# Performance work log

Hardware: AMD Instinct MI355X
Metric: run time of the kernel (lower is better)

Reference implementation:

```python
import jax, jax.numpy as jnp
import numpy as np

N = 200_000           # particles
E = 6_400_000         # neighbor pairs (~32 per particle)
SUPPORT = 0.05
EPS = SUPPORT ** 2 * 0.1
DELTA = 0.1
C0 = 10.0 * float(np.sqrt(2.0 * 9.81 * 0.3))
REST_DENSITY = 1000.0
_KC = 7.0 / float(np.pi)  # 2D Wendland C2 normalization


def kernel_gradient(q, dirs, h):
    # Wendland C2 (2D): W = C/h^2 (1-q)^4 (1+4q), q = r/h in [0,1]
    # dW/dr = C/h^3 * (-20 q (1-q)^3), directed along unit vector dirs
    dkdq = -20.0 * q * (1.0 - q) ** 3 * _KC
    return dirs * (dkdq / h ** 3)[:, None]


def setup_inputs() -> dict:
    key = jax.random.key(0)
    k = jax.random.split(key, 7)
    i = jnp.sort(jax.random.randint(k[0], (E,), 0, N))
    j = jax.random.randint(k[1], (E,), 0, N)
    fluidPosition = jax.random.uniform(k[2], (N, 2), dtype=jnp.float32)
    dx2 = (SUPPORT * 0.5) ** 2
    fluidVolume = dx2 * (1.0 + 0.01 * jax.random.normal(k[3], (N,), dtype=jnp.float32))
    fluidDensity = 0.95 + 0.1 * jax.random.uniform(k[4], (N,), dtype=jnp.float32)
    d = jax.random.normal(k[5], (E, 2), dtype=jnp.float32)
    distances = d / (jnp.linalg.norm(d, axis=1, keepdims=True) + 1e-8)  # unit directions
    radialDistances = jax.random.uniform(k[6], (E,), dtype=jnp.float32, minval=0.05, maxval=1.0)
    return {"fluidPosition": fluidPosition, "fluidVolume": fluidVolume,
            "fluidDensity": fluidDensity, "distances": distances,
            "radialDistances": radialDistances, "i": i, "j": j}


def reference(fluidPosition, fluidVolume, fluidDensity, distances, radialDistances, i, j):
    h = SUPPORT
    n = fluidDensity.shape[0]
    gradW = kernel_gradient(radialDistances, distances, h)          # [E,2]
    r_ba = -distances * (radialDistances * h)[:, None]              # [E,2] displacement
    Vj = fluidVolume[j]

    # --- normalization matrix: sum_j 2 Vj * outer(r_ba, gradW) ---
    term = jnp.einsum('nu,nv->nuv', r_ba, gradW) * (2.0 * Vj)[:, None, None]
    M = jax.ops.segment_sum(term, i, num_segments=n)                # [N,2,2]

    # --- pseudo-inverse + renormalized kernel gradient per edge ---
    Li = jnp.linalg.pinv(M)                                         # [N,2,2]
    grad = jnp.einsum('nuv,nv->nu', Li[i], gradW)                   # [E,2]
    dwij_mag = jnp.sum(jnp.abs(gradW), axis=1)                      # L1 norms
    norm_mag = jnp.sum(jnp.abs(grad), axis=1)
    change = jnp.abs(norm_mag - dwij_mag) / (dwij_mag + 1e-4 * h)
    grad = jnp.where((change < 0.1)[:, None], grad, gradW)

    # --- renormalized density gradient ---
    rho = fluidDensity * REST_DENSITY
    rho_ba = rho[j] - rho[i]
    gradRho = jax.ops.segment_sum((2.0 * rho_ba * Vj)[:, None] * grad, i, num_segments=n)

    # --- deltaSPH density diffusion ---
    rji2 = jnp.sum(r_ba * r_ba, axis=1) + EPS
    densityTerm = 0.5 * jnp.einsum('nu,nu->n', gradRho[i] + gradRho[j], r_ba)
    gradTerm = jnp.einsum('nu,nu->n', gradW, r_ba / rji2[:, None])
    prod = (rho_ba + densityTerm) * gradTerm
    return 2.0 * h * DELTA * C0 * jax.ops.segment_sum(prod * Vj, i, num_segments=n)
```

## Files before the change

### kernel.cpp

```cpp
#include <hip/hip_runtime.h>
#include <math.h>

#define WAVE 64

#define KC        2.2281692032865347f
#define H         0.05f
#define INV_H2    400.0f
#define INV_H3    8000.0f
#define EPS_REF   0.00025f
#define K_OUT     0.24261080f
#define REST_RHO  1000.0f

__device__ __forceinline__ float wendland_dkdq(float q) {
    float omq = 1.0f - q;
    return -20.0f * q * omq * omq * omq * KC;
}

template<int NV>
__device__ __forceinline__ void seg_reduce4(const int k[4], float v[4][NV],
                                            float* __restrict__ base) {
    const int lane = threadIdx.x & (WAVE - 1);
    const int k0 = k[0], k3 = k[3];
    const bool split = (k0 != k3);
    const int firstLen  = (k[1]==k0) ? ((k[2]==k0) ? ((k[3]==k0)?4:3) : 2) : 1;
    const int lastStart = (k[2]==k3) ? ((k[1]==k3) ? ((k[0]==k3)?0:1) : 2) : 3;

    float vin[NV], vfirst[NV];
#pragma unroll
    for (int c = 0; c < NV; ++c) {
        float s = v[3][c];
        if (lastStart <= 2) s += v[2][c];
        if (lastStart <= 1) s += v[1][c];
        if (lastStart == 0) s += v[0][c];
        vin[c] = s;
        float f = v[0][c];
        if (firstLen >= 2) f += v[1][c];
        if (firstLen >= 3) f += v[2][c];
        if (firstLen >= 4) f += v[3][c];
        vfirst[c] = f;
    }

#pragma unroll
    for (int idx = 1; idx <= 2; ++idx) {
        if (idx >= firstLen && idx < lastStart && k[idx] >= 0) {
#pragma unroll
            for (int c = 0; c < NV; ++c)
                atomicAdd(base + (size_t)k[idx] * NV + c, v[idx][c]);
        }
    }

    float S[NV];
#pragma unroll
    for (int c = 0; c < NV; ++c) S[c] = vin[c];
    const int klast = k3;
#pragma unroll
    for (int d = 1; d < WAVE; d <<= 1) {
        int okey = __shfl_up(klast, d, WAVE);
        float ov[NV];
#pragma unroll
        for (int c = 0; c < NV; ++c) ov[c] = __shfl_up(S[c], d, WAVE);
        if (lane >= d && okey == klast) {
#pragma unroll
            for (int c = 0; c < NV; ++c) S[c] += ov[c];
        }
    }

    const int prevk = __shfl_up(klast, 1, WAVE);
    float P[NV];
#pragma unroll
    for (int c = 0; c < NV; ++c) P[c] = __shfl_up(S[c], 1, WAVE);
    if (split && k0 >= 0) {
        const bool carry = (lane > 0 && prevk == k0);
#pragma unroll
        for (int c = 0; c < NV; ++c)
            atomicAdd(base + (size_t)k0 * NV + c, vfirst[c] + (carry ? P[c] : 0.f));
    }

    const int nk0 = __shfl_down(k0, 1, WAVE);
    const bool tail = (lane == WAVE - 1) || (nk0 != klast);
    if (tail && klast >= 0) {
#pragma unroll
        for (int c = 0; c < NV; ++c)
            atomicAdd(base + (size_t)klast * NV + c, S[c]);
    }
}

struct Edge4 {
    int   i[4], j[4];
    float q[4], dx[4], dy[4];
};

__device__ __forceinline__ void load_edge4(int t, int E,
        const int* __restrict__ ei, const int* __restrict__ ej,
        const float* __restrict__ qarr, const float2* __restrict__ dirs, Edge4& ed) {
    const long e0 = 4L * t;
    if (e0 + 3 < (long)E) {
        int4   i4 = ((const int4*)ei)[t];
        int4   j4 = ((const int4*)ej)[t];
        float4 q4 = ((const float4*)qarr)[t];
        float4 dA = ((const float4*)dirs)[2 * t];
        float4 dB = ((const float4*)dirs)[2 * t + 1];
        ed.i[0]=i4.x; ed.i[1]=i4.y; ed.i[2]=i4.z; ed.i[3]=i4.w;
        ed.j[0]=j4.x; ed.j[1]=j4.y; ed.j[2]=j4.z; ed.j[3]=j4.w;
        ed.q[0]=q4.x; ed.q[1]=q4.y; ed.q[2]=q4.z; ed.q[3]=q4.w;
        ed.dx[0]=dA.x; ed.dy[0]=dA.y; ed.dx[1]=dA.z; ed.dy[1]=dA.w;
        ed.dx[2]=dB.x; ed.dy[2]=dB.y; ed.dx[3]=dB.z; ed.dy[3]=dB.w;
    } else {
        int lastk = -1;
#pragma unroll
        for (int u = 0; u < 4; ++u) {
            long e = e0 + u;
            if (e < (long)E) {
                ed.i[u] = ei[e]; ed.j[u] = ej[e]; ed.q[u] = qarr[e];
                float2 d = dirs[e]; ed.dx[u] = d.x; ed.dy[u] = d.y;
                lastk = ed.i[u];
            } else {
                ed.i[u] = lastk; ed.j[u] = 0; ed.q[u] = 0.f;
                ed.dx[u] = 0.f; ed.dy[u] = 0.f;
            }
        }
    }
}

__global__ void k_edge_M4(const float2* __restrict__ dirs, const float* __restrict__ qarr,
                          const int* __restrict__ ei, const int* __restrict__ ej,
                          const float* __restrict__ vol, float* __restrict__ M, int E) {
    int t = blockIdx.x * blockDim.x + threadIdx.x;
    Edge4 ed; load_edge4(t, E, ei, ej, qarr, dirs, ed);
    float vj[4];
#pragma unroll
    for (int u = 0; u < 4; ++u) vj[u] = vol[ed.j[u]];
    int k[4]; float v[4][3];
#pragma unroll
    for (int u = 0; u < 4; ++u) {
        float q = ed.q[u];
        float s = -2.0f * vj[u] * q * wendland_dkdq(q) * INV_H2;
        k[u] = ed.i[u];
        v[u][0] = s * ed.dx[u] * ed.dx[u];
        v[u][1] = s * ed.dx[u] * ed.dy[u];
        v[u][2] = s * ed.dy[u] * ed.dy[u];
    }
    seg_reduce4<3>(k, v, M);
}

__global__ void k_node_pinv_pack(float* __restrict__ M, const float* __restrict__ vol,
                                 const float* __restrict__ dens, float2* __restrict__ vd, int N) {
    int n = blockIdx.x * blockDim.x + threadIdx.x;
    if (n >= N) return;
    vd[n] = make_float2(vol[n], dens[n]);
    float a = M[3*n+0], b = M[3*n+1], c = M[3*n+2];
    float half_tr   = 0.5f * (a + c);
    float half_diff = 0.5f * (a - c);
    float disc = sqrtf(half_diff * half_diff + b * b);
    float l1 = half_tr + disc, l2 = half_tr - disc;
    float smax = fmaxf(fabsf(l1), fabsf(l2));
    float cutoff = 2.3841858e-6f * smax;
    float i00 = 0.f, i01 = 0.f, i11 = 0.f;
    if (fabsf(l2) > cutoff) {
        float inv = 1.0f / (a * c - b * b);
        i00 =  c * inv; i01 = -b * inv; i11 = a * inv;
    } else if (fabsf(l1) > cutoff) {
        float vax = b,      vay = l1 - a;
        float vbx = l1 - c, vby = b;
        float na = vax*vax + vay*vay, nb = vbx*vbx + vby*vby;
        float vx, vy, n2;
        if (nb >= na) { vx = vbx; vy = vby; n2 = nb; }
        else          { vx = vax; vy = vay; n2 = na; }
        float inv = 1.0f / (l1 * n2);
        i00 = vx*vx*inv; i01 = vx*vy*inv; i11 = vy*vy*inv;
    }
    M[3*n+0] = i00; M[3*n+1] = i01; M[3*n+2] = i11;
}

__global__ void k_edge_gradRho4(const float2* __restrict__ dirs, const float* __restrict__ qarr,
                                const int* __restrict__ ei, const int* __restrict__ ej,
                                const float2* __restrict__ vd, const float* __restrict__ Li,
                                float* __restrict__ gradRho, int E) {
    int t = blockIdx.x * blockDim.x + threadIdx.x;
    Edge4 ed; load_edge4(t, E, ei, ej, qarr, dirs, ed);
    float2 vdj[4];
#pragma unroll
    for (int u = 0; u < 4; ++u) vdj[u] = vd[ed.j[u]];
    int k[4]; float v[4][2];
#pragma unroll
    for (int u = 0; u < 4; ++u) {
        int key = ed.i[u];
        k[u] = key;
        v[u][0] = 0.f; v[u][1] = 0.f;
        if (key >= 0) {
            float q = ed.q[u];
            float w = wendland_dkdq(q) * INV_H3;
            float gwx = ed.dx[u] * w, gwy = ed.dy[u] * w;
            float li00 = Li[3*key+0], li01 = Li[3*key+1], li11 = Li[3*key+2];
            float gx = li00 * gwx + li01 * gwy;
            float gy = li01 * gwx + li11 * gwy;
            float dwij_mag = fabsf(gwx) + fabsf(gwy);
            float norm_mag = fabsf(gx) + fabsf(gy);
            float change = fabsf(norm_mag - dwij_mag) / (dwij_mag + 1e-4f * H);
            if (!(change < 0.1f)) { gx = gwx; gy = gwy; }
            float dens_i = vd[key].y;
            float val = 2.0f * REST_RHO * (vdj[u].y - dens_i) * vdj[u].x;
            v[u][0] = val * gx;
            v[u][1] = val * gy;
        }
    }
    seg_reduce4<2>(k, v, gradRho);
}

__global__ void k_pack_nd(const float* __restrict__ vol, const float* __restrict__ dens,
                          const float2* __restrict__ gradRho, float4* __restrict__ nd, int N) {
    int n = blockIdx.x * blockDim.x + threadIdx.x;
    if (n >= N) return;
    float2 g = gradRho[n];
    nd[n] = make_float4(vol[n], dens[n], g.x, g.y);
}

__global__ void k_edge_out4(const float2* __restrict__ dirs, const float* __restrict__ qarr,
                            const int* __restrict__ ei, const int* __restrict__ ej,
                            const float4* __restrict__ nd, float* __restrict__ out, int E) {
    int t = blockIdx.x * blockDim.x + threadIdx.x;
    Edge4 ed; load_edge4(t, E, ei, ej, qarr, dirs, ed);
    float4 ndj[4];
#pragma unroll
    for (int u = 0; u < 4; ++u) ndj[u] = nd[ed.j[u]];
    int k[4]; float v[4][1];
#pragma unroll
    for (int u = 0; u < 4; ++u) {
        int key = ed.i[u];
        k[u] = key;
        v[u][0] = 0.f;
        if (key >= 0) {
            float4 ndi = nd[key];
            float q = ed.q[u];
            float w = wendland_dkdq(q) * INV_H3;
            float gwx = ed.dx[u] * w, gwy = ed.dy[u] * w;
            float rx = -ed.dx[u] * q * H, ry = -ed.dy[u] * q * H;
            float rji2 = rx * rx + ry * ry + EPS_REF;
            float gradTerm = (gwx * rx + gwy * ry) / rji2;
            float densityTerm = 0.5f * ((ndi.z + ndj[u].z) * rx + (ndi.w + ndj[u].w) * ry);
            float rho_ba = REST_RHO * (ndj[u].y - ndi.y);
            v[u][0] = (rho_ba + densityTerm) * gradTerm * ndj[u].x * K_OUT;
        }
    }
    seg_reduce4<1>(k, v, out);
}

extern "C" void kernel_launch(void* const* d_in, const int* in_sizes, int n_in,
                              void* d_out, int out_size, void* d_ws, size_t ws_size,
                              hipStream_t stream) {
    const float*  vol  = (const float*)d_in[1];
    const float*  dens = (const float*)d_in[2];
    const float2* dirs = (const float2*)d_in[3];
    const float*  qarr = (const float*)d_in[4];
    const int*    ei   = (const int*)d_in[5];
    const int*    ej   = (const int*)d_in[6];
    const int N = in_sizes[1];
    const int E = in_sizes[4];

    float*  M       = (float*)d_ws;
    float*  gradRho = M + (size_t)N * 3;
    float2* vd      = (float2*)(M + (size_t)N * 5);
    float4* nd      = (float4*)(M + (size_t)N * 7);
    float*  out     = (float*)d_out;

    hipMemsetAsync(M, 0, (size_t)N * 5 * sizeof(float), stream);
    hipMemsetAsync(out, 0, (size_t)N * sizeof(float), stream);

    const int tb = 256;
    const int T  = (E + 3) / 4;
    const int gE = (T + tb - 1) / tb;
    const int gN = (N + tb - 1) / tb;

    k_edge_M4       <<<gE, tb, 0, stream>>>(dirs, qarr, ei, ej, vol, M, E);
    k_node_pinv_pack<<<gN, tb, 0, stream>>>(M, vol, dens, vd, N);
    k_edge_gradRho4 <<<gE, tb, 0, stream>>>(dirs, qarr, ei, ej, vd, M, gradRho, E);
    k_pack_nd       <<<gN, tb, 0, stream>>>(vol, dens, (const float2*)gradRho, nd, N);
    k_edge_out4     <<<gE, tb, 0, stream>>>(dirs, qarr, ei, ej, nd, out, E);
}
```

Before: 289.6 us.

## Cache per-edge directions and Vj/density-diff as half2 to cut gathers

The first edge pass now also writes per-edge half-precision copies of the unit direction and of (Vj, rho_j - rho_i). Later passes read these streamed 8 bytes per edge instead of the fp32 directions plus random gathers of neighbor volume and density. The pseudo-inverse is stored as float4 for a single aligned load, and the node packing kernels are merged. This trades random gathers and fp32 traffic for extra edge writes and fp16 rounding of directions and volumes. The density differences (up to about 100) also lose precision in half, which may exceed tolerance. A fallback path is used when the workspace is too small.

```diff
diff --git a/kernel.cpp b/kernel.cpp
--- a/kernel.cpp
+++ b/kernel.cpp
@@ -1,4 +1,5 @@
 #include <hip/hip_runtime.h>
+#include <hip/hip_fp16.h>
 #include <math.h>
 
 #define WAVE 64
@@ -15,6 +16,10 @@
     float omq = 1.0f - q;
     return -20.0f * q * omq * omq * omq * KC;
 }
+
+union H2F { __half2 h; float f; };
+__device__ __forceinline__ float   h2_as_f(__half2 h) { H2F u; u.h = h; return u.f; }
+__device__ __forceinline__ __half2 f_as_h2(float f)   { H2F u; u.f = f; return u.h; }
 
 template<int NV>
 __device__ __forceinline__ void seg_reduce4(const int k[4], float v[4][NV],
@@ -39,7 +44,6 @@
         if (firstLen >= 4) f += v[3][c];
         vfirst[c] = f;
     }
-
 #pragma unroll
     for (int idx = 1; idx <= 2; ++idx) {
         if (idx >= firstLen && idx < lastStart && k[idx] >= 0) {
@@ -48,7 +52,6 @@
                 atomicAdd(base + (size_t)k[idx] * NV + c, v[idx][c]);
         }
     }
-
     float S[NV];
 #pragma unroll
     for (int c = 0; c < NV; ++c) S[c] = vin[c];
@@ -64,7 +67,6 @@
             for (int c = 0; c < NV; ++c) S[c] += ov[c];
         }
     }
-
     const int prevk = __shfl_up(klast, 1, WAVE);
     float P[NV];
 #pragma unroll
@@ -75,7 +77,6 @@
         for (int c = 0; c < NV; ++c)
             atomicAdd(base + (size_t)k0 * NV + c, vfirst[c] + (carry ? P[c] : 0.f));
     }
-
     const int nk0 = __shfl_down(k0, 1, WAVE);
     const bool tail = (lane == WAVE - 1) || (nk0 != klast);
     if (tail && klast >= 0) {
@@ -85,69 +86,83 @@
     }
 }
 
-struct Edge4 {
-    int   i[4], j[4];
-    float q[4], dx[4], dy[4];
-};
-
-__device__ __forceinline__ void load_edge4(int t, int E,
-        const int* __restrict__ ei, const int* __restrict__ ej,
-        const float* __restrict__ qarr, const float2* __restrict__ dirs, Edge4& ed) {
-    const long e0 = 4L * t;
+__global__ void k_init(const float* __restrict__ vol, const float* __restrict__ dens,
+                       float2* __restrict__ vd, int N) {
+    int n = blockIdx.x * blockDim.x + threadIdx.x;
+    if (n < N) vd[n] = make_float2(vol[n], dens[n]);
+}
+
+template<bool FULL>
+__global__ void k_A(const int* __restrict__ ei, const int* __restrict__ ej,
+                    const float* __restrict__ qarr, const float2* __restrict__ dirs,
+                    const float2* __restrict__ vd, __half2* __restrict__ ehd,
+                    __half2* __restrict__ vr, float* __restrict__ M, int E) {
+    int t = blockIdx.x * blockDim.x + threadIdx.x;
+    long e0 = 4L * t;
+    int k[4]; float v[4][3];
     if (e0 + 3 < (long)E) {
         int4   i4 = ((const int4*)ei)[t];
         int4   j4 = ((const int4*)ej)[t];
         float4 q4 = ((const float4*)qarr)[t];
         float4 dA = ((const float4*)dirs)[2 * t];
         float4 dB = ((const float4*)dirs)[2 * t + 1];
-        ed.i[0]=i4.x; ed.i[1]=i4.y; ed.i[2]=i4.z; ed.i[3]=i4.w;
-        ed.j[0]=j4.x; ed.j[1]=j4.y; ed.j[2]=j4.z; ed.j[3]=j4.w;
-        ed.q[0]=q4.x; ed.q[1]=q4.y; ed.q[2]=q4.z; ed.q[3]=q4.w;
-        ed.dx[0]=dA.x; ed.dy[0]=dA.y; ed.dx[1]=dA.z; ed.dy[1]=dA.w;
-        ed.dx[2]=dB.x; ed.dy[2]=dB.y; ed.dx[3]=dB.z; ed.dy[3]=dB.w;
+        int   iv[4] = {i4.x, i4.y, i4.z, i4.w};
+        int   jv[4] = {j4.x, j4.y, j4.z, j4.w};
+        float qv[4] = {q4.x, q4.y, q4.z, q4.w};
+        float dxv[4] = {dA.x, dA.z, dB.x, dB.z};
+        float dyv[4] = {dA.y, dA.w, dB.y, dB.w};
+        float2 vdj[4];
+#pragma unroll
+        for (int u = 0; u < 4; ++u) vdj[u] = vd[jv[u]];
+        float4 ehp, vrp;
+#pragma unroll
+        for (int u = 0; u < 4; ++u) {
+            float rhoi = vd[iv[u]].y;
+            float q = qv[u], dx = dxv[u], dy = dyv[u];
+            float Vj = vdj[u].x;
+            float dro = vdj[u].y - rhoi;
+            float s = -2.0f * Vj * q * wendland_dkdq(q) * INV_H2;
+            k[u] = iv[u];
+            v[u][0] = s * dx * dx; v[u][1] = s * dx * dy; v[u][2] = s * dy * dy;
+            if (FULL) {
+                (&ehp.x)[u] = h2_as_f(__floats2half2_rn(dx, dy));
+                (&vrp.x)[u] = h2_as_f(__floats2half2_rn(Vj, dro));
+            }
+        }
+        if (FULL) {
+            ((float4*)ehd)[t] = ehp;
+            ((float4*)vr)[t]  = vrp;
+        }
     } else {
         int lastk = -1;
 #pragma unroll
         for (int u = 0; u < 4; ++u) {
             long e = e0 + u;
             if (e < (long)E) {
-                ed.i[u] = ei[e]; ed.j[u] = ej[e]; ed.q[u] = qarr[e];
-                float2 d = dirs[e]; ed.dx[u] = d.x; ed.dy[u] = d.y;
-                lastk = ed.i[u];
+                int ii = ei[e], jj = ej[e];
+                float q = qarr[e];
+                float2 d = dirs[e];
+                float2 vdj = vd[jj];
+                float dro = vdj.y - vd[ii].y;
+                float s = -2.0f * vdj.x * q * wendland_dkdq(q) * INV_H2;
+                k[u] = ii;
+                v[u][0] = s * d.x * d.x; v[u][1] = s * d.x * d.y; v[u][2] = s * d.y * d.y;
+                if (FULL) {
+                    ehd[e] = __floats2half2_rn(d.x, d.y);
+                    vr[e]  = __floats2half2_rn(vdj.x, dro);
+                }
+                lastk = ii;
             } else {
-                ed.i[u] = lastk; ed.j[u] = 0; ed.q[u] = 0.f;
-                ed.dx[u] = 0.f; ed.dy[u] = 0.f;
-            }
-        }
-    }
-}
-
-__global__ void k_edge_M4(const float2* __restrict__ dirs, const float* __restrict__ qarr,
-                          const int* __restrict__ ei, const int* __restrict__ ej,
-                          const float* __restrict__ vol, float* __restrict__ M, int E) {
-    int t = blockIdx.x * blockDim.x + threadIdx.x;
-    Edge4 ed; load_edge4(t, E, ei, ej, qarr, dirs, ed);
-    float vj[4];
-#pragma unroll
-    for (int u = 0; u < 4; ++u) vj[u] = vol[ed.j[u]];
-    int k[4]; float v[4][3];
-#pragma unroll
-    for (int u = 0; u < 4; ++u) {
-        float q = ed.q[u];
-        float s = -2.0f * vj[u] * q * wendland_dkdq(q) * INV_H2;
-        k[u] = ed.i[u];
-        v[u][0] = s * ed.dx[u] * ed.dx[u];
-        v[u][1] = s * ed.dx[u] * ed.dy[u];
-        v[u][2] = s * ed.dy[u] * ed.dy[u];
+                k[u] = lastk; v[u][0] = v[u][1] = v[u][2] = 0.f;
+            }
+        }
     }
     seg_reduce4<3>(k, v, M);
 }
 
-__global__ void k_node_pinv_pack(float* __restrict__ M, const float* __restrict__ vol,
-                                 const float* __restrict__ dens, float2* __restrict__ vd, int N) {
+__global__ void k_pinv(const float* __restrict__ M, float4* __restrict__ Li4, int N) {
     int n = blockIdx.x * blockDim.x + threadIdx.x;
     if (n >= N) return;
-    vd[n] = make_float2(vol[n], dens[n]);
     float a = M[3*n+0], b = M[3*n+1], c = M[3*n+2];
     float half_tr   = 0.5f * (a + c);
     float half_diff = 0.5f * (a - c);
@@ -169,77 +184,184 @@
         float inv = 1.0f / (l1 * n2);
         i00 = vx*vx*inv; i01 = vx*vy*inv; i11 = vy*vy*inv;
     }
-    M[3*n+0] = i00; M[3*n+1] = i01; M[3*n+2] = i11;
-}
-
-__global__ void k_edge_gradRho4(const float2* __restrict__ dirs, const float* __restrict__ qarr,
-                                const int* __restrict__ ei, const int* __restrict__ ej,
-                                const float2* __restrict__ vd, const float* __restrict__ Li,
-                                float* __restrict__ gradRho, int E) {
+    Li4[n] = make_float4(i00, i01, i11, 0.f);
+}
+
+template<bool FULL>
+__global__ void k_C(const int* __restrict__ ei, const int* __restrict__ ej,
+                    const float* __restrict__ qarr, const float2* __restrict__ dirs,
+                    const __half2* __restrict__ ehd, const __half2* __restrict__ vr,
+                    const float2* __restrict__ vd, const float4* __restrict__ Li4,
+                    float* __restrict__ g, int E) {
     int t = blockIdx.x * blockDim.x + threadIdx.x;
-    Edge4 ed; load_edge4(t, E, ei, ej, qarr, dirs, ed);
-    float2 vdj[4];
-#pragma unroll
-    for (int u = 0; u < 4; ++u) vdj[u] = vd[ed.j[u]];
+    long e0 = 4L * t;
     int k[4]; float v[4][2];
-#pragma unroll
-    for (int u = 0; u < 4; ++u) {
-        int key = ed.i[u];
-        k[u] = key;
-        v[u][0] = 0.f; v[u][1] = 0.f;
-        if (key >= 0) {
-            float q = ed.q[u];
+    if (e0 + 3 < (long)E) {
+        int4   i4 = ((const int4*)ei)[t];
+        float4 q4 = ((const float4*)qarr)[t];
+        int   iv[4] = {i4.x, i4.y, i4.z, i4.w};
+        float qv[4] = {q4.x, q4.y, q4.z, q4.w};
+        float dxv[4], dyv[4], Vjv[4], drov[4];
+        if (FULL) {
+            float4 es = ((const float4*)ehd)[t];
+            float4 vs = ((const float4*)vr)[t];
+#pragma unroll
+            for (int u = 0; u < 4; ++u) {
+                __half2 hd = f_as_h2((&es.x)[u]);
+                __half2 hv = f_as_h2((&vs.x)[u]);
+                dxv[u] = __low2float(hd);  dyv[u] = __high2float(hd);
+                Vjv[u] = __low2float(hv);  drov[u] = __high2float(hv);
+            }
+        } else {
+            int4   j4 = ((const int4*)ej)[t];
+            float4 dA = ((const float4*)dirs)[2 * t];
+            float4 dB = ((const float4*)dirs)[2 * t + 1];
+            int jv[4] = {j4.x, j4.y, j4.z, j4.w};
+            dxv[0]=dA.x; dyv[0]=dA.y; dxv[1]=dA.z; dyv[1]=dA.w;
+            dxv[2]=dB.x; dyv[2]=dB.y; dxv[3]=dB.z; dyv[3]=dB.w;
+#pragma unroll
+            for (int u = 0; u < 4; ++u) {
+                float2 vdj = vd[jv[u]];
+                Vjv[u] = vdj.x; drov[u] = vdj.y - vd[iv[u]].y;
+            }
+        }
+#pragma unroll
+        for (int u = 0; u < 4; ++u) {
+            int key = iv[u]; k[u] = key;
+            float q = qv[u];
             float w = wendland_dkdq(q) * INV_H3;
-            float gwx = ed.dx[u] * w, gwy = ed.dy[u] * w;
-            float li00 = Li[3*key+0], li01 = Li[3*key+1], li11 = Li[3*key+2];
-            float gx = li00 * gwx + li01 * gwy;
-            float gy = li01 * gwx + li11 * gwy;
+            float gwx = dxv[u] * w, gwy = dyv[u] * w;
+            float4 L = Li4[key];
+            float gx = L.x * gwx + L.y * gwy;
+            float gy = L.y * gwx + L.z * gwy;
             float dwij_mag = fabsf(gwx) + fabsf(gwy);
             float norm_mag = fabsf(gx) + fabsf(gy);
             float change = fabsf(norm_mag - dwij_mag) / (dwij_mag + 1e-4f * H);
             if (!(change < 0.1f)) { gx = gwx; gy = gwy; }
-            float dens_i = vd[key].y;
-            float val = 2.0f * REST_RHO * (vdj[u].y - dens_i) * vdj[u].x;
+            float val = 2.0f * REST_RHO * drov[u] * Vjv[u];
             v[u][0] = val * gx;
             v[u][1] = val * gy;
         }
-    }
-    seg_reduce4<2>(k, v, gradRho);
-}
-
-__global__ void k_pack_nd(const float* __restrict__ vol, const float* __restrict__ dens,
-                          const float2* __restrict__ gradRho, float4* __restrict__ nd, int N) {
-    int n = blockIdx.x * blockDim.x + threadIdx.x;
-    if (n >= N) return;
-    float2 g = gradRho[n];
-    nd[n] = make_float4(vol[n], dens[n], g.x, g.y);
-}
-
-__global__ void k_edge_out4(const float2* __restrict__ dirs, const float* __restrict__ qarr,
-                            const int* __restrict__ ei, const int* __restrict__ ej,
-                            const float4* __restrict__ nd, float* __restrict__ out, int E) {
+    } else {
+        int lastk = -1;
+#pragma unroll
+        for (int u = 0; u < 4; ++u) {
+            long e = e0 + u;
+            v[u][0] = v[u][1] = 0.f;
+            if (e < (long)E) {
+                int key = ei[e]; lastk = key; k[u] = key;
+                float q = qarr[e];
+                float dx, dy, Vj, dro;
+                if (FULL) {
+                    __half2 hd = ehd[e], hv = vr[e];
+                    dx = __low2float(hd); dy = __high2float(hd);
+                    Vj = __low2float(hv); dro = __high2float(hv);
+                } else {
+                    float2 d = dirs[e]; dx = d.x; dy = d.y;
+                    float2 vdj = vd[ej[e]];
+                    Vj = vdj.x; dro = vdj.y - vd[key].y;
+                }
+                float w = wendland_dkdq(q) * INV_H3;
+                float gwx = dx * w, gwy = dy * w;
+                float4 L = Li4[key];
+                float gx = L.x * gwx + L.y * gwy;
+                float gy = L.y * gwx + L.z * gwy;
+                float dwij_mag = fabsf(gwx) + fabsf(gwy);
+                float norm_mag = fabsf(gx) + fabsf(gy);
+                float change = fabsf(norm_mag - dwij_mag) / (dwij_mag + 1e-4f * H);
+                if (!(change < 0.1f)) { gx = gwx; gy = gwy; }
+                float val = 2.0f * REST_RHO * dro * Vj;
+                v[u][0] = val * gx; v[u][1] = val * gy;
+            } else k[u] = lastk;
+        }
+    }
+    seg_reduce4<2>(k, v, g);
+}
+
+template<bool FULL>
+__global__ void k_D(const int* __restrict__ ei, const int* __restrict__ ej,
+                    const float* __restrict__ qarr, const float2* __restrict__ dirs,
+                    const __half2* __restrict__ ehd, const __half2* __restrict__ vr,
+                    const float2* __restrict__ vd, const float2* __restrict__ g,
+                    float* __restrict__ out, int E) {
     int t = blockIdx.x * blockDim.x + threadIdx.x;
-    Edge4 ed; load_edge4(t, E, ei, ej, qarr, dirs, ed);
-    float4 ndj[4];
-#pragma unroll
-    for (int u = 0; u < 4; ++u) ndj[u] = nd[ed.j[u]];
+    long e0 = 4L * t;
     int k[4]; float v[4][1];
-#pragma unroll
-    for (int u = 0; u < 4; ++u) {
-        int key = ed.i[u];
-        k[u] = key;
-        v[u][0] = 0.f;
-        if (key >= 0) {
-            float4 ndi = nd[key];
-            float q = ed.q[u];
+    if (e0 + 3 < (long)E) {
+        int4   i4 = ((const int4*)ei)[t];
+        int4   j4 = ((const int4*)ej)[t];
+        float4 q4 = ((const float4*)qarr)[t];
+        int   iv[4] = {i4.x, i4.y, i4.z, i4.w};
+        int   jv[4] = {j4.x, j4.y, j4.z, j4.w};
+        float qv[4] = {q4.x, q4.y, q4.z, q4.w};
+        float dxv[4], dyv[4], Vjv[4], drov[4];
+        if (FULL) {
+            float4 es = ((const float4*)ehd)[t];
+            float4 vs = ((const float4*)vr)[t];
+#pragma unroll
+            for (int u = 0; u < 4; ++u) {
+                __half2 hd = f_as_h2((&es.x)[u]);
+                __half2 hv = f_as_h2((&vs.x)[u]);
+                dxv[u] = __low2float(hd);  dyv[u] = __high2float(hd);
+                Vjv[u] = __low2float(hv);  drov[u] = __high2float(hv);
+            }
+        } else {
+            float4 dA = ((const float4*)dirs)[2 * t];
+            float4 dB = ((const float4*)dirs)[2 * t + 1];
+            dxv[0]=dA.x; dyv[0]=dA.y; dxv[1]=dA.z; dyv[1]=dA.w;
+            dxv[2]=dB.x; dyv[2]=dB.y; dxv[3]=dB.z; dyv[3]=dB.w;
+#pragma unroll
+            for (int u = 0; u < 4; ++u) {
+                float2 vdj = vd[jv[u]];
+                Vjv[u] = vdj.x; drov[u] = vdj.y - vd[iv[u]].y;
+            }
+        }
+        float2 gjv[4];
+#pragma unroll
+        for (int u = 0; u < 4; ++u) gjv[u] = g[jv[u]];
+#pragma unroll
+        for (int u = 0; u < 4; ++u) {
+            int key = iv[u]; k[u] = key;
+            float2 gi = g[key];
+            float q = qv[u];
             float w = wendland_dkdq(q) * INV_H3;
-            float gwx = ed.dx[u] * w, gwy = ed.dy[u] * w;
-            float rx = -ed.dx[u] * q * H, ry = -ed.dy[u] * q * H;
+            float gwx = dxv[u] * w, gwy = dyv[u] * w;
+            float rx = -dxv[u] * q * H, ry = -dyv[u] * q * H;
             float rji2 = rx * rx + ry * ry + EPS_REF;
             float gradTerm = (gwx * rx + gwy * ry) / rji2;
-            float densityTerm = 0.5f * ((ndi.z + ndj[u].z) * rx + (ndi.w + ndj[u].w) * ry);
-            float rho_ba = REST_RHO * (ndj[u].y - ndi.y);
-            v[u][0] = (rho_ba + densityTerm) * gradTerm * ndj[u].x * K_OUT;
+            float densityTerm = 0.5f * ((gi.x + gjv[u].x) * rx + (gi.y + gjv[u].y) * ry);
+            float rho_ba = REST_RHO * drov[u];
+            v[u][0] = (rho_ba + densityTerm) * gradTerm * Vjv[u] * K_OUT;
+        }
+    } else {
+        int lastk = -1;
+#pragma unroll
+        for (int u = 0; u < 4; ++u) {
+            long e = e0 + u;
+            v[u][0] = 0.f;
+            if (e < (long)E) {
+                int key = ei[e], jj = ej[e]; lastk = key; k[u] = key;
+                float q = qarr[e];
+                float dx, dy, Vj, dro;
+                if (FULL) {
+                    __half2 hd = ehd[e], hv = vr[e];
+                    dx = __low2float(hd); dy = __high2float(hd);
+                    Vj = __low2float(hv); dro = __high2float(hv);
+                } else {
+                    float2 d = dirs[e]; dx = d.x; dy = d.y;
+                    float2 vdj = vd[jj];
+                    Vj = vdj.x; dro = vdj.y - vd[key].y;
+                }
+                float2 gi = g[key], gj = g[jj];
+                float w = wendland_dkdq(q) * INV_H3;
+                float gwx = dx * w, gwy = dy * w;
+                float rx = -dx * q * H, ry = -dy * q * H;
+                float rji2 = rx * rx + ry * ry + EPS_REF;
+                float gradTerm = (gwx * rx + gwy * ry) / rji2;
+                float densityTerm = 0.5f * ((gi.x + gj.x) * rx + (gi.y + gj.y) * ry);
+                float rho_ba = REST_RHO * dro;
+                v[u][0] = (rho_ba + densityTerm) * gradTerm * Vj * K_OUT;
+            } else k[u] = lastk;
         }
     }
     seg_reduce4<1>(k, v, out);
@@ -257,23 +379,36 @@
     const int N = in_sizes[1];
     const int E = in_sizes[4];
 
-    float*  M       = (float*)d_ws;
-    float*  gradRho = M + (size_t)N * 3;
-    float2* vd      = (float2*)(M + (size_t)N * 5);
-    float4* nd      = (float4*)(M + (size_t)N * 7);
-    float*  out     = (float*)d_out;
-
-    hipMemsetAsync(M, 0, (size_t)N * 5 * sizeof(float), stream);
-    hipMemsetAsync(out, 0, (size_t)N * sizeof(float), stream);
+    size_t off = 0;
+    auto alloc = [&](size_t bytes) { void* r = (char*)d_ws + off;
+                                     off = (off + bytes + 15) & ~(size_t)15; return r; };
+    float2*  vd  = (float2*) alloc((size_t)N * 8);
+    float*   M   = (float*)  alloc((size_t)N * 12);
+    float4*  Li4 = (float4*) alloc((size_t)N * 16);
+    __half2* ehd = (__half2*)alloc((size_t)E * 4);
+    __half2* vr  = (__half2*)alloc((size_t)E * 4);
+    const bool full = (off <= ws_size);
+    float2*  g   = full ? vd : (float2*)M;
+    float*   out = (float*)d_out;
 
     const int tb = 256;
-    const int T  = (E + 3) / 4;
-    const int gE = (T + tb - 1) / tb;
     const int gN = (N + tb - 1) / tb;
-
-    k_edge_M4       <<<gE, tb, 0, stream>>>(dirs, qarr, ei, ej, vol, M, E);
-    k_node_pinv_pack<<<gN, tb, 0, stream>>>(M, vol, dens, vd, N);
-    k_edge_gradRho4 <<<gE, tb, 0, stream>>>(dirs, qarr, ei, ej, vd, M, gradRho, E);
-    k_pack_nd       <<<gN, tb, 0, stream>>>(vol, dens, (const float2*)gradRho, nd, N);
-    k_edge_out4     <<<gE, tb, 0, stream>>>(dirs, qarr, ei, ej, nd, out, E);
-}
+    const int gT = ((E + 3) / 4 + tb - 1) / tb;
+
+    k_init<<<gN, tb, 0, stream>>>(vol, dens, vd, N);
+    hipMemsetAsync(M, 0, (size_t)N * 12, stream);
+    hipMemsetAsync(out, 0, (size_t)N * 4, stream);
+    if (full) {
+        k_A<true><<<gT, tb, 0, stream>>>(ei, ej, qarr, dirs, vd, ehd, vr, M, E);
+        k_pinv<<<gN, tb, 0, stream>>>(M, Li4, N);
+        hipMemsetAsync(g, 0, (size_t)N * 8, stream);
+        k_C<true><<<gT, tb, 0, stream>>>(ei, ej, qarr, dirs, ehd, vr, vd, Li4, (float*)g, E);
+        k_D<true><<<gT, tb, 0, stream>>>(ei, ej, qarr, dirs, ehd, vr, vd, g, out, E);
+    } else {
+        k_A<false><<<gT, tb, 0, stream>>>(ei, ej, qarr, dirs, vd, ehd, vr, M, E);
+        k_pinv<<<gN, tb, 0, stream>>>(M, Li4, N);
+        hipMemsetAsync(g, 0, (size_t)N * 8, stream);
+        k_C<false><<<gT, tb, 0, stream>>>(ei, ej, qarr, dirs, ehd, vr, vd, Li4, (float*)g, E);
+        k_D<false><<<gT, tb, 0, stream>>>(ei, ej, qarr, dirs, ehd, vr, vd, g, out, E);
+    }
+}
```

Result: faster. 255.0 us (-12.0%).

## Fuse M, pinv and gradRho into node-blocked CSR kernel with shared-memory reductions

Applied to the files above, without the earlier changes.

Builds a CSR row pointer from the sorted i array, then has each block own 32 particles and walk their edge range. M accumulation, pseudo-inverse and gradRho reduction happen in one kernel using shared-memory atomics, and the first chunks of per-edge data are cached in registers for reuse between the two passes. This removes the global atomics, the memsets and the intermediate node kernels, and cuts edge re-reads. In exchange it adds a rowptr prep pass and extra block syncs, and per-block load balance now depends on how many edges each 32-particle group has.

```diff
diff --git a/kernel.cpp b/kernel.cpp
--- a/kernel.cpp
+++ b/kernel.cpp
@@ -1,7 +1,10 @@
 #include <hip/hip_runtime.h>
 #include <math.h>
 
-#define WAVE 64
+#define WAVE   64
+#define NPB    32
+#define BLOCKT 256
+#define SMAX   2
 
 #define KC        2.2281692032865347f
 #define H         0.05f
@@ -12,13 +15,12 @@
 #define REST_RHO  1000.0f
 
 __device__ __forceinline__ float wendland_dkdq(float q) {
-    float omq = 1.0f - q;
-    return -20.0f * q * omq * omq * omq * KC;
+    float o = 1.f - q;
+    return -20.f * q * o * o * o * KC;
 }
 
 template<int NV>
-__device__ __forceinline__ void seg_reduce4(const int k[4], float v[4][NV],
-                                            float* __restrict__ base) {
+__device__ __forceinline__ void seg_reduce4(const int k[4], float v[4][NV], float* base) {
     const int lane = threadIdx.x & (WAVE - 1);
     const int k0 = k[0], k3 = k[3];
     const bool split = (k0 != k3);
@@ -39,7 +41,6 @@
         if (firstLen >= 4) f += v[3][c];
         vfirst[c] = f;
     }
-
 #pragma unroll
     for (int idx = 1; idx <= 2; ++idx) {
         if (idx >= firstLen && idx < lastStart && k[idx] >= 0) {
@@ -48,7 +49,6 @@
                 atomicAdd(base + (size_t)k[idx] * NV + c, v[idx][c]);
         }
     }
-
     float S[NV];
 #pragma unroll
     for (int c = 0; c < NV; ++c) S[c] = vin[c];
@@ -64,7 +64,6 @@
             for (int c = 0; c < NV; ++c) S[c] += ov[c];
         }
     }
-
     const int prevk = __shfl_up(klast, 1, WAVE);
     float P[NV];
 #pragma unroll
@@ -75,7 +74,6 @@
         for (int c = 0; c < NV; ++c)
             atomicAdd(base + (size_t)k0 * NV + c, vfirst[c] + (carry ? P[c] : 0.f));
     }
-
     const int nk0 = __shfl_down(k0, 1, WAVE);
     const bool tail = (lane == WAVE - 1) || (nk0 != klast);
     if (tail && klast >= 0) {
@@ -85,164 +83,257 @@
     }
 }
 
-struct Edge4 {
-    int   i[4], j[4];
-    float q[4], dx[4], dy[4];
-};
-
-__device__ __forceinline__ void load_edge4(int t, int E,
+struct EW { int iv[4], jv[4]; float qv[4], dxv[4], dyv[4]; bool okv[4]; };
+
+__device__ __forceinline__ void load_win(long e0, int beg, int end, int E,
         const int* __restrict__ ei, const int* __restrict__ ej,
-        const float* __restrict__ qarr, const float2* __restrict__ dirs, Edge4& ed) {
-    const long e0 = 4L * t;
+        const float* __restrict__ qarr, const float2* __restrict__ dirs, EW& w) {
     if (e0 + 3 < (long)E) {
-        int4   i4 = ((const int4*)ei)[t];
-        int4   j4 = ((const int4*)ej)[t];
-        float4 q4 = ((const float4*)qarr)[t];
-        float4 dA = ((const float4*)dirs)[2 * t];
-        float4 dB = ((const float4*)dirs)[2 * t + 1];
-        ed.i[0]=i4.x; ed.i[1]=i4.y; ed.i[2]=i4.z; ed.i[3]=i4.w;
-        ed.j[0]=j4.x; ed.j[1]=j4.y; ed.j[2]=j4.z; ed.j[3]=j4.w;
-        ed.q[0]=q4.x; ed.q[1]=q4.y; ed.q[2]=q4.z; ed.q[3]=q4.w;
-        ed.dx[0]=dA.x; ed.dy[0]=dA.y; ed.dx[1]=dA.z; ed.dy[1]=dA.w;
-        ed.dx[2]=dB.x; ed.dy[2]=dB.y; ed.dx[3]=dB.z; ed.dy[3]=dB.w;
+        int4   i4 = *(const int4*)(ei + e0);
+        int4   j4 = *(const int4*)(ej + e0);
+        float4 q4 = *(const float4*)(qarr + e0);
+        float4 dA = *(const float4*)((const float*)dirs + 2 * e0);
+        float4 dB = *(const float4*)((const float*)dirs + 2 * e0 + 4);
+        w.iv[0]=i4.x; w.iv[1]=i4.y; w.iv[2]=i4.z; w.iv[3]=i4.w;
+        w.jv[0]=j4.x; w.jv[1]=j4.y; w.jv[2]=j4.z; w.jv[3]=j4.w;
+        w.qv[0]=q4.x; w.qv[1]=q4.y; w.qv[2]=q4.z; w.qv[3]=q4.w;
+        w.dxv[0]=dA.x; w.dyv[0]=dA.y; w.dxv[1]=dA.z; w.dyv[1]=dA.w;
+        w.dxv[2]=dB.x; w.dyv[2]=dB.y; w.dxv[3]=dB.z; w.dyv[3]=dB.w;
     } else {
-        int lastk = -1;
 #pragma unroll
         for (int u = 0; u < 4; ++u) {
             long e = e0 + u;
             if (e < (long)E) {
-                ed.i[u] = ei[e]; ed.j[u] = ej[e]; ed.q[u] = qarr[e];
-                float2 d = dirs[e]; ed.dx[u] = d.x; ed.dy[u] = d.y;
-                lastk = ed.i[u];
-            } else {
-                ed.i[u] = lastk; ed.j[u] = 0; ed.q[u] = 0.f;
-                ed.dx[u] = 0.f; ed.dy[u] = 0.f;
-            }
-        }
-    }
-}
-
-__global__ void k_edge_M4(const float2* __restrict__ dirs, const float* __restrict__ qarr,
-                          const int* __restrict__ ei, const int* __restrict__ ej,
-                          const float* __restrict__ vol, float* __restrict__ M, int E) {
-    int t = blockIdx.x * blockDim.x + threadIdx.x;
-    Edge4 ed; load_edge4(t, E, ei, ej, qarr, dirs, ed);
-    float vj[4];
-#pragma unroll
-    for (int u = 0; u < 4; ++u) vj[u] = vol[ed.j[u]];
-    int k[4]; float v[4][3];
+                w.iv[u] = ei[e]; w.jv[u] = ej[e]; w.qv[u] = qarr[e];
+                float2 d = dirs[e]; w.dxv[u] = d.x; w.dyv[u] = d.y;
+            } else { w.iv[u]=0; w.jv[u]=0; w.qv[u]=0.f; w.dxv[u]=0.f; w.dyv[u]=0.f; }
+        }
+    }
 #pragma unroll
     for (int u = 0; u < 4; ++u) {
-        float q = ed.q[u];
-        float s = -2.0f * vj[u] * q * wendland_dkdq(q) * INV_H2;
-        k[u] = ed.i[u];
-        v[u][0] = s * ed.dx[u] * ed.dx[u];
-        v[u][1] = s * ed.dx[u] * ed.dy[u];
-        v[u][2] = s * ed.dy[u] * ed.dy[u];
-    }
-    seg_reduce4<3>(k, v, M);
-}
-
-__global__ void k_node_pinv_pack(float* __restrict__ M, const float* __restrict__ vol,
-                                 const float* __restrict__ dens, float2* __restrict__ vd, int N) {
-    int n = blockIdx.x * blockDim.x + threadIdx.x;
-    if (n >= N) return;
-    vd[n] = make_float2(vol[n], dens[n]);
-    float a = M[3*n+0], b = M[3*n+1], c = M[3*n+2];
-    float half_tr   = 0.5f * (a + c);
-    float half_diff = 0.5f * (a - c);
-    float disc = sqrtf(half_diff * half_diff + b * b);
-    float l1 = half_tr + disc, l2 = half_tr - disc;
-    float smax = fmaxf(fabsf(l1), fabsf(l2));
-    float cutoff = 2.3841858e-6f * smax;
-    float i00 = 0.f, i01 = 0.f, i11 = 0.f;
-    if (fabsf(l2) > cutoff) {
-        float inv = 1.0f / (a * c - b * b);
-        i00 =  c * inv; i01 = -b * inv; i11 = a * inv;
-    } else if (fabsf(l1) > cutoff) {
-        float vax = b,      vay = l1 - a;
-        float vbx = l1 - c, vby = b;
-        float na = vax*vax + vay*vay, nb = vbx*vbx + vby*vby;
-        float vx, vy, n2;
-        if (nb >= na) { vx = vbx; vy = vby; n2 = nb; }
-        else          { vx = vax; vy = vay; n2 = na; }
-        float inv = 1.0f / (l1 * n2);
-        i00 = vx*vx*inv; i01 = vx*vy*inv; i11 = vy*vy*inv;
-    }
-    M[3*n+0] = i00; M[3*n+1] = i01; M[3*n+2] = i11;
-}
-
-__global__ void k_edge_gradRho4(const float2* __restrict__ dirs, const float* __restrict__ qarr,
-                                const int* __restrict__ ei, const int* __restrict__ ej,
-                                const float2* __restrict__ vd, const float* __restrict__ Li,
-                                float* __restrict__ gradRho, int E) {
-    int t = blockIdx.x * blockDim.x + threadIdx.x;
-    Edge4 ed; load_edge4(t, E, ei, ej, qarr, dirs, ed);
-    float2 vdj[4];
-#pragma unroll
-    for (int u = 0; u < 4; ++u) vdj[u] = vd[ed.j[u]];
-    int k[4]; float v[4][2];
-#pragma unroll
-    for (int u = 0; u < 4; ++u) {
-        int key = ed.i[u];
-        k[u] = key;
-        v[u][0] = 0.f; v[u][1] = 0.f;
-        if (key >= 0) {
-            float q = ed.q[u];
-            float w = wendland_dkdq(q) * INV_H3;
-            float gwx = ed.dx[u] * w, gwy = ed.dy[u] * w;
-            float li00 = Li[3*key+0], li01 = Li[3*key+1], li11 = Li[3*key+2];
-            float gx = li00 * gwx + li01 * gwy;
-            float gy = li01 * gwx + li11 * gwy;
-            float dwij_mag = fabsf(gwx) + fabsf(gwy);
-            float norm_mag = fabsf(gx) + fabsf(gy);
-            float change = fabsf(norm_mag - dwij_mag) / (dwij_mag + 1e-4f * H);
-            if (!(change < 0.1f)) { gx = gwx; gy = gwy; }
-            float dens_i = vd[key].y;
-            float val = 2.0f * REST_RHO * (vdj[u].y - dens_i) * vdj[u].x;
-            v[u][0] = val * gx;
-            v[u][1] = val * gy;
-        }
-    }
-    seg_reduce4<2>(k, v, gradRho);
-}
-
-__global__ void k_pack_nd(const float* __restrict__ vol, const float* __restrict__ dens,
-                          const float2* __restrict__ gradRho, float4* __restrict__ nd, int N) {
-    int n = blockIdx.x * blockDim.x + threadIdx.x;
-    if (n >= N) return;
-    float2 g = gradRho[n];
-    nd[n] = make_float4(vol[n], dens[n], g.x, g.y);
-}
-
-__global__ void k_edge_out4(const float2* __restrict__ dirs, const float* __restrict__ qarr,
-                            const int* __restrict__ ei, const int* __restrict__ ej,
-                            const float4* __restrict__ nd, float* __restrict__ out, int E) {
-    int t = blockIdx.x * blockDim.x + threadIdx.x;
-    Edge4 ed; load_edge4(t, E, ei, ej, qarr, dirs, ed);
-    float4 ndj[4];
-#pragma unroll
-    for (int u = 0; u < 4; ++u) ndj[u] = nd[ed.j[u]];
-    int k[4]; float v[4][1];
-#pragma unroll
-    for (int u = 0; u < 4; ++u) {
-        int key = ed.i[u];
-        k[u] = key;
-        v[u][0] = 0.f;
-        if (key >= 0) {
-            float4 ndi = nd[key];
-            float q = ed.q[u];
-            float w = wendland_dkdq(q) * INV_H3;
-            float gwx = ed.dx[u] * w, gwy = ed.dy[u] * w;
-            float rx = -ed.dx[u] * q * H, ry = -ed.dy[u] * q * H;
-            float rji2 = rx * rx + ry * ry + EPS_REF;
-            float gradTerm = (gwx * rx + gwy * ry) / rji2;
-            float densityTerm = 0.5f * ((ndi.z + ndj[u].z) * rx + (ndi.w + ndj[u].w) * ry);
-            float rho_ba = REST_RHO * (ndj[u].y - ndi.y);
-            v[u][0] = (rho_ba + densityTerm) * gradTerm * ndj[u].x * K_OUT;
-        }
-    }
-    seg_reduce4<1>(k, v, out);
+        long e = e0 + u;
+        w.okv[u] = (e >= (long)beg) && (e < (long)end) && (e < (long)E);
+    }
+}
+
+__global__ void k_prep(const int* __restrict__ ei, const float* __restrict__ vol,
+                       const float* __restrict__ dens, int* __restrict__ rowptr,
+                       float2* __restrict__ vd, int N, int E) {
+    int e = blockIdx.x * blockDim.x + threadIdx.x;
+    if (e <= E) {
+        int prev = (e == 0) ? -1 : ei[e - 1];
+        int cur  = (e == E) ? N  : ei[e];
+        for (int t = prev + 1; t <= cur; ++t) rowptr[t] = e;
+    }
+    if (e < N) vd[e] = make_float2(vol[e], dens[e]);
+}
+
+__global__ __launch_bounds__(BLOCKT, 4)
+void k_AC(const int* __restrict__ ei, const int* __restrict__ ej,
+          const float* __restrict__ qarr, const float2* __restrict__ dirs,
+          const float2* __restrict__ vd, const int* __restrict__ rowptr,
+          float4* __restrict__ nd, int N, int E) {
+    __shared__ float  Mld[NPB * 3];
+    __shared__ float  Lild[NPB * 3];
+    __shared__ float  gld[NPB * 2];
+    __shared__ float2 vdl[NPB];
+    const int tid = threadIdx.x;
+    const int n0  = blockIdx.x * NPB;
+    const int nHi = min(n0 + NPB, N);
+    if (tid < NPB && n0 + tid < N) vdl[tid] = vd[n0 + tid];
+    if (tid < NPB * 3) Mld[tid] = 0.f;
+    if (tid < NPB * 2) gld[tid] = 0.f;
+    __syncthreads();
+    const int  beg  = rowptr[n0], end = rowptr[nHi];
+    const long beg4 = (long)beg & ~3L;
+    const int  waveBase = tid & ~(WAVE - 1);
+
+    int   li_s[4 * SMAX];
+    float w_s[4 * SMAX], dx_s[4 * SMAX], dy_s[4 * SMAX], val_s[4 * SMAX];
+#pragma unroll
+    for (int x = 0; x < 4 * SMAX; ++x) { li_s[x] = -1; w_s[x]=dx_s[x]=dy_s[x]=val_s[x]=0.f; }
+
+#pragma unroll
+    for (int c = 0; c < SMAX; ++c) {
+        long ebw = beg4 + ((long)c * BLOCKT + waveBase) * 4;
+        if (ebw < (long)end) {
+            long e0 = beg4 + ((long)c * BLOCKT + tid) * 4;
+            EW wd; load_win(e0, beg, end, E, ei, ej, qarr, dirs, wd);
+            int k[4]; float v[4][3];
+#pragma unroll
+            for (int u = 0; u < 4; ++u) {
+                k[u] = -1; v[u][0] = v[u][1] = v[u][2] = 0.f;
+                if (wd.okv[u]) {
+                    int li = wd.iv[u] - n0;
+                    float q = wd.qv[u], dx = wd.dxv[u], dy = wd.dyv[u];
+                    float2 vdj = vd[wd.jv[u]];
+                    float wq = wendland_dkdq(q);
+                    float s = -2.f * vdj.x * q * wq * INV_H2;
+                    k[u] = li;
+                    v[u][0] = s * dx * dx; v[u][1] = s * dx * dy; v[u][2] = s * dy * dy;
+                    li_s[c*4+u] = li; w_s[c*4+u] = wq * INV_H3;
+                    dx_s[c*4+u] = dx; dy_s[c*4+u] = dy;
+                    val_s[c*4+u] = 2.f * REST_RHO * (vdj.y - vdl[li].y) * vdj.x;
+                }
+            }
+            seg_reduce4<3>(k, v, Mld);
+        }
+    }
+    for (int c = SMAX; ; ++c) {
+        long ebw = beg4 + ((long)c * BLOCKT + waveBase) * 4;
+        if (ebw >= (long)end) break;
+        long e0 = beg4 + ((long)c * BLOCKT + tid) * 4;
+        EW wd; load_win(e0, beg, end, E, ei, ej, qarr, dirs, wd);
+        int k[4]; float v[4][3];
+#pragma unroll
+        for (int u = 0; u < 4; ++u) {
+            k[u] = -1; v[u][0] = v[u][1] = v[u][2] = 0.f;
+            if (wd.okv[u]) {
+                int li = wd.iv[u] - n0;
+                float q = wd.qv[u], dx = wd.dxv[u], dy = wd.dyv[u];
+                float2 vdj = vd[wd.jv[u]];
+                float s = -2.f * vdj.x * q * wendland_dkdq(q) * INV_H2;
+                k[u] = li;
+                v[u][0] = s * dx * dx; v[u][1] = s * dx * dy; v[u][2] = s * dy * dy;
+            }
+        }
+        seg_reduce4<3>(k, v, Mld);
+    }
+    __syncthreads();
+
+    if (tid < NPB) {
+        float a = Mld[3*tid], b = Mld[3*tid+1], cc = Mld[3*tid+2];
+        float half_tr   = 0.5f * (a + cc);
+        float half_diff = 0.5f * (a - cc);
+        float disc = sqrtf(half_diff * half_diff + b * b);
+        float l1 = half_tr + disc, l2 = half_tr - disc;
+        float smax = fmaxf(fabsf(l1), fabsf(l2));
+        float cutoff = 2.3841858e-6f * smax;
+        float i00 = 0.f, i01 = 0.f, i11 = 0.f;
+        if (fabsf(l2) > cutoff) {
+            float inv = 1.0f / (a * cc - b * b);
+            i00 =  cc * inv; i01 = -b * inv; i11 = a * inv;
+        } else if (fabsf(l1) > cutoff) {
+            float vax = b,       vay = l1 - a;
+            float vbx = l1 - cc, vby = b;
+            float na = vax*vax + vay*vay, nb = vbx*vbx + vby*vby;
+            float vx, vy, n2;
+            if (nb >= na) { vx = vbx; vy = vby; n2 = nb; }
+            else          { vx = vax; vy = vay; n2 = na; }
+            float inv = 1.0f / (l1 * n2);
+            i00 = vx*vx*inv; i01 = vx*vy*inv; i11 = vy*vy*inv;
+        }
+        Lild[3*tid] = i00; Lild[3*tid+1] = i01; Lild[3*tid+2] = i11;
+    }
+    __syncthreads();
+
+#pragma unroll
+    for (int c = 0; c < SMAX; ++c) {
+        long ebw = beg4 + ((long)c * BLOCKT + waveBase) * 4;
+        if (ebw < (long)end) {
+            int k[4]; float v[4][2];
+#pragma unroll
+            for (int u = 0; u < 4; ++u) {
+                int li = li_s[c*4+u];
+                k[u] = li; v[u][0] = v[u][1] = 0.f;
+                if (li >= 0) {
+                    float w = w_s[c*4+u], dx = dx_s[c*4+u], dy = dy_s[c*4+u];
+                    float gwx = dx * w, gwy = dy * w;
+                    float L0 = Lild[3*li], L1 = Lild[3*li+1], L2v = Lild[3*li+2];
+                    float gx = L0 * gwx + L1 * gwy;
+                    float gy = L1 * gwx + L2v * gwy;
+                    float dm = fabsf(gwx) + fabsf(gwy);
+                    float nm = fabsf(gx) + fabsf(gy);
+                    float change = fabsf(nm - dm) / (dm + 1e-4f * H);
+                    if (!(change < 0.1f)) { gx = gwx; gy = gwy; }
+                    v[u][0] = val_s[c*4+u] * gx;
+                    v[u][1] = val_s[c*4+u] * gy;
+                }
+            }
+            seg_reduce4<2>(k, v, gld);
+        }
+    }
+    for (int c = SMAX; ; ++c) {
+        long ebw = beg4 + ((long)c * BLOCKT + waveBase) * 4;
+        if (ebw >= (long)end) break;
+        long e0 = beg4 + ((long)c * BLOCKT + tid) * 4;
+        EW wd; load_win(e0, beg, end, E, ei, ej, qarr, dirs, wd);
+        int k[4]; float v[4][2];
+#pragma unroll
+        for (int u = 0; u < 4; ++u) {
+            k[u] = -1; v[u][0] = v[u][1] = 0.f;
+            if (wd.okv[u]) {
+                int li = wd.iv[u] - n0;
+                float q = wd.qv[u], dx = wd.dxv[u], dy = wd.dyv[u];
+                float2 vdj = vd[wd.jv[u]];
+                float w = wendland_dkdq(q) * INV_H3;
+                float gwx = dx * w, gwy = dy * w;
+                float L0 = Lild[3*li], L1 = Lild[3*li+1], L2v = Lild[3*li+2];
+                float gx = L0 * gwx + L1 * gwy;
+                float gy = L1 * gwx + L2v * gwy;
+                float dm = fabsf(gwx) + fabsf(gwy);
+                float nm = fabsf(gx) + fabsf(gy);
+                float change = fabsf(nm - dm) / (dm + 1e-4f * H);
+                if (!(change < 0.1f)) { gx = gwx; gy = gwy; }
+                float val = 2.f * REST_RHO * (vdj.y - vdl[li].y) * vdj.x;
+                k[u] = li; v[u][0] = val * gx; v[u][1] = val * gy;
+            }
+        }
+        seg_reduce4<2>(k, v, gld);
+    }
+    __syncthreads();
+    if (tid < NPB && n0 + tid < N)
+        nd[n0 + tid] = make_float4(vdl[tid].x, vdl[tid].y, gld[2*tid], gld[2*tid+1]);
+}
+
+__global__ __launch_bounds__(BLOCKT, 4)
+void k_D(const int* __restrict__ ei, const int* __restrict__ ej,
+         const float* __restrict__ qarr, const float2* __restrict__ dirs,
+         const float4* __restrict__ nd, const int* __restrict__ rowptr,
+         float* __restrict__ out, int N, int E) {
+    __shared__ float4 ndl[NPB];
+    __shared__ float  outl[NPB];
+    const int tid = threadIdx.x;
+    const int n0  = blockIdx.x * NPB;
+    const int nHi = min(n0 + NPB, N);
+    if (tid < NPB && n0 + tid < N) ndl[tid] = nd[n0 + tid];
+    if (tid < NPB) outl[tid] = 0.f;
+    __syncthreads();
+    const int  beg  = rowptr[n0], end = rowptr[nHi];
+    const long beg4 = (long)beg & ~3L;
+    const int  waveBase = tid & ~(WAVE - 1);
+
+    for (int c = 0; ; ++c) {
+        long ebw = beg4 + ((long)c * BLOCKT + waveBase) * 4;
+        if (ebw >= (long)end) break;
+        long e0 = beg4 + ((long)c * BLOCKT + tid) * 4;
+        EW wd; load_win(e0, beg, end, E, ei, ej, qarr, dirs, wd);
+        float4 ndj[4];
+#pragma unroll
+        for (int u = 0; u < 4; ++u) ndj[u] = wd.okv[u] ? nd[wd.jv[u]] : make_float4(0,0,0,0);
+        int k[4]; float v[4][1];
+#pragma unroll
+        for (int u = 0; u < 4; ++u) {
+            k[u] = -1; v[u][0] = 0.f;
+            if (wd.okv[u]) {
+                int li = wd.iv[u] - n0;
+                float4 ndi = ndl[li];
+                float q = wd.qv[u], dx = wd.dxv[u], dy = wd.dyv[u];
+                float w = wendland_dkdq(q) * INV_H3;
+                float gwx = dx * w, gwy = dy * w;
+                float rx = -dx * q * H, ry = -dy * q * H;
+                float rji2 = rx * rx + ry * ry + EPS_REF;
+                float gradTerm = (gwx * rx + gwy * ry) / rji2;
+                float densityTerm = 0.5f * ((ndi.z + ndj[u].z) * rx + (ndi.w + ndj[u].w) * ry);
+                float rho_ba = REST_RHO * (ndj[u].y - ndi.y);
+                k[u] = li;
+                v[u][0] = (rho_ba + densityTerm) * gradTerm * ndj[u].x;
+            }
+        }
+        seg_reduce4<1>(k, v, outl);
+    }
+    __syncthreads();
+    if (tid < NPB && n0 + tid < N) out[n0 + tid] = outl[tid] * K_OUT;
 }
 
 extern "C" void kernel_launch(void* const* d_in, const int* in_sizes, int n_in,
@@ -257,23 +348,17 @@
     const int N = in_sizes[1];
     const int E = in_sizes[4];
 
-    float*  M       = (float*)d_ws;
-    float*  gradRho = M + (size_t)N * 3;
-    float2* vd      = (float2*)(M + (size_t)N * 5);
-    float4* nd      = (float4*)(M + (size_t)N * 7);
-    float*  out     = (float*)d_out;
-
-    hipMemsetAsync(M, 0, (size_t)N * 5 * sizeof(float), stream);
-    hipMemsetAsync(out, 0, (size_t)N * sizeof(float), stream);
+    char*   p      = (char*)d_ws;
+    int*    rowptr = (int*)p;      p += (((size_t)(N + 1) * 4) + 15) & ~(size_t)15;
+    float2* vd     = (float2*)p;   p += (size_t)N * sizeof(float2);
+    float4* nd     = (float4*)p;
+    float*  out    = (float*)d_out;
 
     const int tb = 256;
-    const int T  = (E + 3) / 4;
-    const int gE = (T + tb - 1) / tb;
-    const int gN = (N + tb - 1) / tb;
-
-    k_edge_M4       <<<gE, tb, 0, stream>>>(dirs, qarr, ei, ej, vol, M, E);
-    k_node_pinv_pack<<<gN, tb, 0, stream>>>(M, vol, dens, vd, N);
-    k_edge_gradRho4 <<<gE, tb, 0, stream>>>(dirs, qarr, ei, ej, vd, M, gradRho, E);
-    k_pack_nd       <<<gN, tb, 0, stream>>>(vol, dens, (const float2*)gradRho, nd, N);
-    k_edge_out4     <<<gE, tb, 0, stream>>>(dirs, qarr, ei, ej, nd, out, E);
-}
+    const int gP = (E + 1 + tb - 1) / tb;
+    const int gB = (N + NPB - 1) / NPB;
+
+    k_prep<<<gP, tb, 0, stream>>>(ei, vol, dens, rowptr, vd, N, E);
+    k_AC  <<<gB, BLOCKT, 0, stream>>>(ei, ej, qarr, dirs, vd, rowptr, nd, N, E);
+    k_D   <<<gB, BLOCKT, 0, stream>>>(ei, ej, qarr, dirs, nd, rowptr, out, N, E);
+}
```

After: 247.2 us. 14.7% less time.
